# Performance work log

Hardware: AMD Instinct MI355X
Metric: run time of the kernel (lower is better)

Reference implementation:

```python
import jax, jax.numpy as jnp
import numpy as np

S = 64.0   # scale (default s)
M = 0.5    # angular margin (default m)
EPS = 1e-07
N, D, C = 2048, 128, 100000

def setup_inputs() -> dict:
    key = jax.random.key(0)
    kx, kw, kl = jax.random.split(key, 3)
    x = jax.random.normal(kx, (N, D), dtype=jnp.float32)
    # NOTE: the torch module never actually normalizes W (local rebinding bug),
    # so W is a raw linear weight. Small init keeps exp(s*wf) finite.
    W = jax.random.normal(kw, (C, D), dtype=jnp.float32) * 0.01
    labels = jax.random.randint(kl, (N,), 0, C, dtype=jnp.int64)
    return {"x": x, "W": W, "labels": labels}

def reference(x, W, labels):
    # L2-normalize embeddings only (matches original: weight normalize is a no-op)
    x_n = x / jnp.linalg.norm(x, axis=1, keepdims=True)
    wf = jnp.einsum('nd,cd->nc', x_n, W)                      # [N, C] logits
    tgt = jnp.take_along_axis(wf, labels[:, None], axis=1)[:, 0]  # wf[i, y_i]
    tgt = jnp.clip(tgt, -1.0 + EPS, 1.0 - EPS)
    numerator = S * jnp.cos(jnp.arccos(tgt) + M)              # margin logit
    # sum over j != y_i of exp(s * wf_ij)
    exp_all = jnp.exp(S * wf)
    excl_sum = jnp.sum(exp_all, axis=1) - jnp.take_along_axis(exp_all, labels[:, None], axis=1)[:, 0]
    denominator = jnp.exp(numerator) + excl_sum
    L = numerator - jnp.log(denominator)
    return -jnp.mean(L)
```

## Files before the change

kernel.cpp:

```cpp
#include <hip/hip_runtime.h>
#include <math.h>

typedef __attribute__((ext_vector_type(8))) short s16x8;
typedef __attribute__((ext_vector_type(4))) float f32x4;

#define N_ROWS 2048
#define D_DIM  128
#define N_CLS  100000
#define N_TILES 782
#define N_PAD   96.0f
#define S_SCALE 64.0f
#define S_LOG2E 92.33248261689366f
#define EPS_F   1e-7f
#define COS_M   0.8775825618903728f
#define SIN_M   0.479425538604203f

#if __has_builtin(__builtin_amdgcn_exp2f)
#define EXP2F(x) __builtin_amdgcn_exp2f(x)
#else
#define EXP2F(x) exp2f(x)
#endif

__device__ __forceinline__ unsigned int f2bf1(float f) {
    unsigned int u = __float_as_uint(f);
    return (u + 0x7FFFu + ((u >> 16) & 1u)) >> 16;
}
__device__ __forceinline__ unsigned int f2bf2(float lo, float hi) {
    return f2bf1(lo) | (f2bf1(hi) << 16);
}

__global__ __launch_bounds__(256)
void k_normalize(const float* __restrict__ x, const float* __restrict__ W,
                 const int* __restrict__ labels,
                 float* __restrict__ tgt, uint4* __restrict__ xb2) {
    const int t = threadIdx.x;
    const int row = blockIdx.x * 32 + (t >> 3);
    const int p = t & 7;

    const f32x4* src = (const f32x4*)(x + (size_t)row * D_DIM + p * 16);
    f32x4 v[4];
    float s = 0.f;
    #pragma unroll
    for (int q = 0; q < 4; q++) {
        v[q] = src[q];
        s += v[q][0]*v[q][0] + v[q][1]*v[q][1] + v[q][2]*v[q][2] + v[q][3]*v[q][3];
    }
    s += __shfl_xor(s, 1); s += __shfl_xor(s, 2); s += __shfl_xor(s, 4);
    const float inv = 1.0f / sqrtf(s);

    const int y = labels[row];
    const f32x4* wsrc = (const f32x4*)(W + (size_t)y * D_DIM + p * 16);
    float d = 0.f;
    #pragma unroll
    for (int q = 0; q < 4; q++) {
        f32x4 w = wsrc[q];
        d += v[q][0]*w[0] + v[q][1]*w[1] + v[q][2]*w[2] + v[q][3]*w[3];
    }
    d += __shfl_xor(d, 1); d += __shfl_xor(d, 2); d += __shfl_xor(d, 4);
    if (p == 0) tgt[row] = d * inv;

    const float invs = inv * S_LOG2E;
    #pragma unroll
    for (int q = 0; q < 4; q++) {
        v[q][0] *= invs; v[q][1] *= invs; v[q][2] *= invs; v[q][3] *= invs;
    }

    const int gt = row >> 7, rr = row & 127;
    const int wn = rr >> 6, j = (rr >> 4) & 3, lrr = rr & 15;
    #pragma unroll
    for (int c2 = 0; c2 < 2; c2++) {
        const int ck = p * 2 + c2;
        const int ks = ck >> 2, lk = ck & 3;
        const int idx = gt * 2048 + wn * 1024 + j * 256 + ks * 64 + lk * 16 + lrr;
        f32x4 f0 = v[c2 * 2], f1 = v[c2 * 2 + 1];
        xb2[idx] = make_uint4(f2bf2(f0[0], f0[1]), f2bf2(f0[2], f0[3]),
                              f2bf2(f1[0], f1[1]), f2bf2(f1[2], f1[3]));
    }
}

#define MFMA16(ACC, BUF) do {                                                 \
    ACC##0 = (f32x4){0.f,0.f,0.f,0.f}; ACC##1 = (f32x4){0.f,0.f,0.f,0.f};     \
    ACC##2 = (f32x4){0.f,0.f,0.f,0.f}; ACC##3 = (f32x4){0.f,0.f,0.f,0.f};     \
    _Pragma("unroll")                                                         \
    for (int ks_ = 0; ks_ < 4; ks_++) {                                       \
        const s16x8 b_ = *(const s16x8*)&BUF[ks_];                            \
        ACC##0 = __builtin_amdgcn_mfma_f32_16x16x32_bf16(a_[ks_][0], b_, ACC##0, 0, 0, 0); \
        ACC##1 = __builtin_amdgcn_mfma_f32_16x16x32_bf16(a_[ks_][1], b_, ACC##1, 0, 0, 0); \
        ACC##2 = __builtin_amdgcn_mfma_f32_16x16x32_bf16(a_[ks_][2], b_, ACC##2, 0, 0, 0); \
        ACC##3 = __builtin_amdgcn_mfma_f32_16x16x32_bf16(a_[ks_][3], b_, ACC##3, 0, 0, 0); \
    }                                                                         \
} while (0)

#define RELOAD(BUF, J) do {                                                   \
    if (it < 15) {                                                            \
        _Pragma("unroll")                                                     \
        for (int ks_ = 0; ks_ < 4; ks_++)                                     \
            BUF[ks_] = bbase[(it + 1) * 2048 + (J) * 256 + ks_ * 64];         \
    }                                                                         \
} while (0)

#define EXPST(ACC, ITE, JE) do {                                              \
    f32x4 pv;                                                                 \
    _Pragma("unroll")                                                         \
    for (int r_ = 0; r_ < 4; r_++)                                            \
        pv[r_] = (EXP2F(ACC##0[r_]) + EXP2F(ACC##1[r_]))                      \
               + (EXP2F(ACC##2[r_]) + EXP2F(ACC##3[r_]));                     \
    float pj = (pv[0] + pv[1]) + (pv[2] + pv[3]);                             \
    pj += __shfl_xor(pj, 16);                                                 \
    pj += __shfl_xor(pj, 32);                                                 \
    if ((lane >> 4) == 0)                                                     \
        atomicAdd(&psum[ITE][wn * 64 + (JE) * 16 + lr], pj);                  \
} while (0)

__global__ __launch_bounds__(256, 3)
void k_main(const uint4* __restrict__ xb2, const float* __restrict__ W,
            float* __restrict__ rowsum) {
    __shared__ uint4 Wsh[2048];
    __shared__ float psum[16][128];
    const int t = threadIdx.x;
    const int c0 = blockIdx.x * 128;

    #pragma unroll
    for (int k = 0; k < 8; k++) ((float*)psum)[t + k * 256] = 0.f;

    #pragma unroll
    for (int m = 0; m < 8; m++) {
        const int idx = m * 256 + t;
        const int flr = idx & 15, lk = (idx >> 4) & 3;
        const int ks = (idx >> 6) & 3, fi = (idx >> 8) & 3, fwm = idx >> 10;
        const int cls = c0 + fwm * 64 + fi * 16 + flr;
        const int k0 = (ks * 4 + lk) * 8;
        uint4 val = make_uint4(0u, 0u, 0u, 0u);
        if (cls < N_CLS) {
            const f32x4* g = (const f32x4*)(W + (size_t)cls * D_DIM + k0);
            f32x4 f0 = g[0], f1 = g[1];
            val.x = f2bf2(f0[0], f0[1]); val.y = f2bf2(f0[2], f0[3]);
            val.z = f2bf2(f1[0], f1[1]); val.w = f2bf2(f1[2], f1[3]);
        }
        Wsh[idx] = val;
    }
    __syncthreads();

    const int lane = t & 63;
    const int wid = t >> 6;
    const int wm = wid >> 1;
    const int wn = wid & 1;
    const int lr = lane & 15;
    const uint4* bbase = xb2 + wn * 1024 + lane;

    uint4 b0[4], b1[4], b2[4], b3[4];
    s16x8 a_[4][4];
    f32x4 accA0, accA1, accA2, accA3;
    f32x4 accB0, accB1, accB2, accB3;

    #pragma unroll
    for (int ks = 0; ks < 4; ks++) {
        b0[ks] = bbase[0 * 256 + ks * 64];
        b1[ks] = bbase[1 * 256 + ks * 64];
        b2[ks] = bbase[2 * 256 + ks * 64];
        b3[ks] = bbase[3 * 256 + ks * 64];
    }

    for (int it = 0; it < 16; it++) {
        #pragma unroll
        for (int ks = 0; ks < 4; ks++)
            #pragma unroll
            for (int i = 0; i < 4; i++)
                a_[ks][i] = *(const s16x8*)&Wsh[wm * 1024 + i * 256 + ks * 64 + lane];
        if (it) EXPST(accB, it - 1, 3);
        MFMA16(accA, b0);  RELOAD(b0, 0);
        MFMA16(accB, b1);  RELOAD(b1, 1);  EXPST(accA, it, 0);
        MFMA16(accA, b2);  RELOAD(b2, 2);  EXPST(accB, it, 1);
        MFMA16(accB, b3);  RELOAD(b3, 3);  EXPST(accA, it, 2);
    }
    EXPST(accB, 15, 3);

    __syncthreads();
    #pragma unroll
    for (int k = 0; k < 8; k++) {
        const int flat = t + k * 256;
        const int it = flat >> 7, r = flat & 127;
        atomicAdd(&rowsum[it * 128 + r], psum[it][r]);
    }
}

__global__ void k_final(const float* __restrict__ rowsum, const float* __restrict__ tgt,
                        float* __restrict__ out) {
    int t = threadIdx.x;
    float lsum = 0.f;
    for (int i = t; i < N_ROWS; i += 256) {
        float tr = tgt[i];
        float tc = fminf(fmaxf(tr, -1.f + EPS_F), 1.f - EPS_F);
        float num = S_SCALE * (tc * COS_M - sqrtf(fmaxf(1.f - tc * tc, 0.f)) * SIN_M);
        float excl = rowsum[i] - N_PAD - __expf(S_SCALE * tr);
        float den = __expf(num) + excl;
        lsum += num - logf(den);
    }
    #pragma unroll
    for (int off = 1; off < 64; off <<= 1) lsum += __shfl_xor(lsum, off);
    __shared__ float wsums[4];
    if ((t & 63) == 0) wsums[t >> 6] = lsum;
    __syncthreads();
    if (t == 0) out[0] = -(wsums[0] + wsums[1] + wsums[2] + wsums[3]) / (float)N_ROWS;
}

extern "C" void kernel_launch(void* const* d_in, const int* in_sizes, int n_in,
                              void* d_out, int out_size, void* d_ws, size_t ws_size,
                              hipStream_t stream) {
    const float* x = (const float*)d_in[0];
    const float* W = (const float*)d_in[1];
    const int* labels = (const int*)d_in[2];
    float* out = (float*)d_out;

    uint4* xb2    = (uint4*)d_ws;
    float* rowsum = (float*)((char*)xb2 + (size_t)N_ROWS * D_DIM * 2);
    float* tgt    = rowsum + N_ROWS;

    hipMemsetAsync(rowsum, 0, N_ROWS * sizeof(float), stream);
    k_normalize<<<N_ROWS / 32, 256, 0, stream>>>(x, W, labels, tgt, xb2);
    k_main<<<N_TILES, 256, 0, stream>>>(xb2, W, rowsum);
    k_final<<<1, 256, 0, stream>>>(rowsum, tgt, out);
}
```

Measured before the change: 93.67 us.

## Restructure main GEMM loop into 64-row steps with split-K double buffering

The main kernel now walks the row dimension in 32 steps of 64 rows instead of 16 steps of 128. Each wave covers a 64x32 tile with 8 accumulators, and the x fragments are double-buffered across the two K halves rather than holding four full 128-row buffers. The aim is to cut register pressure enough to raise the occupancy target from 3 to 4 blocks per CU. In exchange, the software pipelining that overlapped the exp/reduce of one tile with the MFMAs of the next is dropped, leaving less intra-wave overlap.

```diff
diff --git a/kernel.cpp b/kernel.cpp
--- a/kernel.cpp
+++ b/kernel.cpp
@@ -78,45 +78,11 @@
     }
 }
 
-#define MFMA16(ACC, BUF) do {                                                 \
-    ACC##0 = (f32x4){0.f,0.f,0.f,0.f}; ACC##1 = (f32x4){0.f,0.f,0.f,0.f};     \
-    ACC##2 = (f32x4){0.f,0.f,0.f,0.f}; ACC##3 = (f32x4){0.f,0.f,0.f,0.f};     \
-    _Pragma("unroll")                                                         \
-    for (int ks_ = 0; ks_ < 4; ks_++) {                                       \
-        const s16x8 b_ = *(const s16x8*)&BUF[ks_];                            \
-        ACC##0 = __builtin_amdgcn_mfma_f32_16x16x32_bf16(a_[ks_][0], b_, ACC##0, 0, 0, 0); \
-        ACC##1 = __builtin_amdgcn_mfma_f32_16x16x32_bf16(a_[ks_][1], b_, ACC##1, 0, 0, 0); \
-        ACC##2 = __builtin_amdgcn_mfma_f32_16x16x32_bf16(a_[ks_][2], b_, ACC##2, 0, 0, 0); \
-        ACC##3 = __builtin_amdgcn_mfma_f32_16x16x32_bf16(a_[ks_][3], b_, ACC##3, 0, 0, 0); \
-    }                                                                         \
-} while (0)
-
-#define RELOAD(BUF, J) do {                                                   \
-    if (it < 15) {                                                            \
-        _Pragma("unroll")                                                     \
-        for (int ks_ = 0; ks_ < 4; ks_++)                                     \
-            BUF[ks_] = bbase[(it + 1) * 2048 + (J) * 256 + ks_ * 64];         \
-    }                                                                         \
-} while (0)
-
-#define EXPST(ACC, ITE, JE) do {                                              \
-    f32x4 pv;                                                                 \
-    _Pragma("unroll")                                                         \
-    for (int r_ = 0; r_ < 4; r_++)                                            \
-        pv[r_] = (EXP2F(ACC##0[r_]) + EXP2F(ACC##1[r_]))                      \
-               + (EXP2F(ACC##2[r_]) + EXP2F(ACC##3[r_]));                     \
-    float pj = (pv[0] + pv[1]) + (pv[2] + pv[3]);                             \
-    pj += __shfl_xor(pj, 16);                                                 \
-    pj += __shfl_xor(pj, 32);                                                 \
-    if ((lane >> 4) == 0)                                                     \
-        atomicAdd(&psum[ITE][wn * 64 + (JE) * 16 + lr], pj);                  \
-} while (0)
-
-__global__ __launch_bounds__(256, 3)
+__global__ __launch_bounds__(256, 4)
 void k_main(const uint4* __restrict__ xb2, const float* __restrict__ W,
             float* __restrict__ rowsum) {
     __shared__ uint4 Wsh[2048];
-    __shared__ float psum[16][128];
+    __shared__ float psum[32][64];
     const int t = threadIdx.x;
     const int c0 = blockIdx.x * 128;
 
@@ -144,43 +110,87 @@
     const int lane = t & 63;
     const int wid = t >> 6;
     const int wm = wid >> 1;
-    const int wn = wid & 1;
+    const int rh = wid & 1;
     const int lr = lane & 15;
-    const uint4* bbase = xb2 + wn * 1024 + lane;
-
-    uint4 b0[4], b1[4], b2[4], b3[4];
-    s16x8 a_[4][4];
-    f32x4 accA0, accA1, accA2, accA3;
-    f32x4 accB0, accB1, accB2, accB3;
-
-    #pragma unroll
-    for (int ks = 0; ks < 4; ks++) {
-        b0[ks] = bbase[0 * 256 + ks * 64];
-        b1[ks] = bbase[1 * 256 + ks * 64];
-        b2[ks] = bbase[2 * 256 + ks * 64];
-        b3[ks] = bbase[3 * 256 + ks * 64];
-    }
-
-    for (int it = 0; it < 16; it++) {
-        #pragma unroll
-        for (int ks = 0; ks < 4; ks++)
+    const uint4* bbase = xb2 + rh * 512 + lane;
+
+    uint4 bE[4], bO[4];
+    s16x8 a_[2][4];
+
+    #pragma unroll
+    for (int jj = 0; jj < 2; jj++)
+        #pragma unroll
+        for (int ks = 0; ks < 2; ks++)
+            bE[jj * 2 + ks] = bbase[jj * 256 + ks * 64];
+
+    for (int it = 0; it < 32; it++) {
+        f32x4 acc[4][2];
+        #pragma unroll
+        for (int i = 0; i < 4; i++)
+            #pragma unroll
+            for (int jj = 0; jj < 2; jj++)
+                acc[i][jj] = (f32x4){0.f, 0.f, 0.f, 0.f};
+
+        #pragma unroll
+        for (int jj = 0; jj < 2; jj++)
+            #pragma unroll
+            for (int ks = 0; ks < 2; ks++)
+                bO[jj * 2 + ks] = bbase[it * 1024 + jj * 256 + (ks + 2) * 64];
+        #pragma unroll
+        for (int ks = 0; ks < 2; ks++)
             #pragma unroll
             for (int i = 0; i < 4; i++)
                 a_[ks][i] = *(const s16x8*)&Wsh[wm * 1024 + i * 256 + ks * 64 + lane];
-        if (it) EXPST(accB, it - 1, 3);
-        MFMA16(accA, b0);  RELOAD(b0, 0);
-        MFMA16(accB, b1);  RELOAD(b1, 1);  EXPST(accA, it, 0);
-        MFMA16(accA, b2);  RELOAD(b2, 2);  EXPST(accB, it, 1);
-        MFMA16(accB, b3);  RELOAD(b3, 3);  EXPST(accA, it, 2);
-    }
-    EXPST(accB, 15, 3);
+        #pragma unroll
+        for (int ks = 0; ks < 2; ks++)
+            #pragma unroll
+            for (int i = 0; i < 4; i++)
+                #pragma unroll
+                for (int jj = 0; jj < 2; jj++)
+                    acc[i][jj] = __builtin_amdgcn_mfma_f32_16x16x32_bf16(
+                        a_[ks][i], *(const s16x8*)&bE[jj * 2 + ks], acc[i][jj], 0, 0, 0);
+
+        if (it < 31) {
+            #pragma unroll
+            for (int jj = 0; jj < 2; jj++)
+                #pragma unroll
+                for (int ks = 0; ks < 2; ks++)
+                    bE[jj * 2 + ks] = bbase[(it + 1) * 1024 + jj * 256 + ks * 64];
+        }
+        #pragma unroll
+        for (int ks = 0; ks < 2; ks++)
+            #pragma unroll
+            for (int i = 0; i < 4; i++)
+                a_[ks][i] = *(const s16x8*)&Wsh[wm * 1024 + i * 256 + (ks + 2) * 64 + lane];
+        #pragma unroll
+        for (int ks = 0; ks < 2; ks++)
+            #pragma unroll
+            for (int i = 0; i < 4; i++)
+                #pragma unroll
+                for (int jj = 0; jj < 2; jj++)
+                    acc[i][jj] = __builtin_amdgcn_mfma_f32_16x16x32_bf16(
+                        a_[ks][i], *(const s16x8*)&bO[jj * 2 + ks], acc[i][jj], 0, 0, 0);
+
+        #pragma unroll
+        for (int jj = 0; jj < 2; jj++) {
+            f32x4 pv;
+            #pragma unroll
+            for (int r = 0; r < 4; r++)
+                pv[r] = (EXP2F(acc[0][jj][r]) + EXP2F(acc[1][jj][r]))
+                      + (EXP2F(acc[2][jj][r]) + EXP2F(acc[3][jj][r]));
+            float pj = (pv[0] + pv[1]) + (pv[2] + pv[3]);
+            pj += __shfl_xor(pj, 16);
+            pj += __shfl_xor(pj, 32);
+            if ((lane >> 4) == 0)
+                atomicAdd(&psum[it][rh * 32 + jj * 16 + lr], pj);
+        }
+    }
 
     __syncthreads();
     #pragma unroll
     for (int k = 0; k < 8; k++) {
         const int flat = t + k * 256;
-        const int it = flat >> 7, r = flat & 127;
-        atomicAdd(&rowsum[it * 128 + r], psum[it][r]);
+        atomicAdd(&rowsum[flat], ((const float*)psum)[flat]);
     }
 }
 
```

New measurement: 93.96 us. No clear change (+0.3%).
